# Kernel tuning notes

Measured on AMD Instinct MI355X. Metric: run time of the kernel, lower is better.

## Reference

```python
import jax, jax.numpy as jnp
import numpy as np
from jax import lax

B = 256
C1 = 256          # conv1 channels
NUM_CAPS = 32     # primary capsule types
CAP_DIM = 8       # primary capsule dim
NUM_PRIMARY = NUM_CAPS * 6 * 6  # 1152
NUM_OUT = 10
OUT_DIM = 16
NUM_ROUTING = 3


def squash(v):
    # v: (..., d)
    sq = jnp.sum(v * v, axis=-1, keepdims=True)
    scale = sq / (1.0 + sq)
    return scale * v / jnp.sqrt(sq + 1e-8)


def setup_inputs() -> dict:
    key = jax.random.key(0)
    k = jax.random.split(key, 6)
    x = jax.random.normal(k[0], (B, 1, 28, 28), dtype=jnp.float32)
    # kaiming fan_out init for convs
    conv1_w = jax.random.normal(k[1], (C1, 1, 9, 9), dtype=jnp.float32) * np.sqrt(2.0 / (C1 * 81))
    conv1_b = jnp.zeros((C1,), dtype=jnp.float32)
    pc_out = NUM_CAPS * CAP_DIM  # 256
    pc_w = jax.random.normal(k[2], (pc_out, C1, 9, 9), dtype=jnp.float32) * np.sqrt(2.0 / (pc_out * 81))
    pc_b = jnp.zeros((pc_out,), dtype=jnp.float32)
    W_digit = jax.random.normal(k[3], (NUM_PRIMARY, CAP_DIM, NUM_OUT, OUT_DIM), dtype=jnp.float32) * 0.01
    return {"x": x, "conv1_w": conv1_w, "conv1_b": conv1_b,
            "pc_w": pc_w, "pc_b": pc_b, "W_digit": W_digit}


def _conv(x, w, b, stride):
    y = lax.conv_general_dilated(x, w, (stride, stride), 'VALID',
                                 dimension_numbers=('NCHW', 'OIHW', 'NCHW'))
    return y + b[None, :, None, None]


def reference(x, conv1_w, conv1_b, pc_w, pc_b, W_digit):
    # conv1 + ReLU: (B,1,28,28) -> (B,256,20,20)
    h = jax.nn.relu(_conv(x, conv1_w, conv1_b, 1))
    # primary caps conv: -> (B, 256, 6, 6)
    p = _conv(h, pc_w, pc_b, 2)
    bsz, _, oh, ow = p.shape
    # (B, num_caps, cap_dim, H, W) -> (B, num_caps, H, W, cap_dim) -> (B, N, d)
    p = p.reshape(bsz, NUM_CAPS, CAP_DIM, oh, ow)
    p = jnp.transpose(p, (0, 1, 3, 4, 2)).reshape(bsz, NUM_CAPS * oh * ow, CAP_DIM)
    u = squash(p)  # (B, 1152, 8)
    # dynamic routing
    u_hat = jnp.einsum('bid,idjo->bijo', u, W_digit)  # (B, 1152, 10, 16)
    b_logits = jnp.zeros((bsz, NUM_PRIMARY, NUM_OUT, 1), dtype=u_hat.dtype)
    v = None
    for it in range(NUM_ROUTING):
        c = jax.nn.softmax(b_logits, axis=2)
        s = jnp.sum(c * u_hat, axis=1)          # (B, 10, 16)
        v = squash(s)
        if it < NUM_ROUTING - 1:
            agreement = jnp.sum(u_hat * v[:, None, :, :], axis=-1, keepdims=True)
            b_logits = b_logits + agreement
    return v
```

## Files before the change

### kernel.cpp

```cpp
#include <hip/hip_runtime.h>
#include <hip/hip_bf16.h>

#define NI 1152

typedef __attribute__((ext_vector_type(8))) _Float16 f16x8;
typedef __attribute__((ext_vector_type(4))) float f32x4;
typedef __attribute__((ext_vector_type(8))) unsigned short u16x8;
typedef __attribute__((ext_vector_type(4))) unsigned short u16x4;

static const size_t UHAT_OFF = 0;
static const size_t W6_OFF   = 0;
static const size_t H3_OFF   = 10750976UL;
static const size_t WT1_OFF  = 63179776UL;
static const size_t PP_OFF   = 94371840UL;
static const size_t SP_OFF   = 103809024UL;
static const size_t L_OFF    = 127401984UL;
static const size_t V_OFF    = 139198464UL;

__device__ __forceinline__ unsigned short f2bf(float x) {
    unsigned u = __builtin_bit_cast(unsigned, x);
    u += 0x7fffu + ((u >> 16) & 1u);
    return (unsigned short)(u >> 16);
}
__device__ __forceinline__ float bf2f(unsigned short h) {
    return __builtin_bit_cast(float, (unsigned)h << 16);
}
__device__ __forceinline__ void atomAddF(float* p, float v) {
    __hip_atomic_fetch_add(p, v, __ATOMIC_RELAXED, __HIP_MEMORY_SCOPE_AGENT);
}

#define GLD16(gsrc, ldst)                                                      \
    __builtin_amdgcn_global_load_lds(                                          \
        (__attribute__((address_space(1))) const void*)(gsrc),                 \
        (__attribute__((address_space(3))) void*)(ldst), 16, 0, 0)

__global__ __launch_bounds__(256) void k_prep_w(const float* __restrict__ pcw,
                                                _Float16* __restrict__ w6) {
    __shared__ float sl[5184];
    int oc  = blockIdx.x;
    int ic0 = blockIdx.y * 64;
    const float* src = pcw + (size_t)oc * 20736 + (size_t)ic0 * 81;
    for (int j = threadIdx.x; j < 5184; j += 256) sl[j] = src[j];
    __syncthreads();
    int og = oc >> 4, fr = oc & 15;
    for (int t = threadIdx.x; t < 5184; t += 256) {
        int tap = t >> 6, i = t & 63;
        int ic = ic0 + i;
        int ks = ic >> 5, kch = (ic >> 3) & 3, icl = ic & 7;
        int lane = kch * 16 + fr;
        w6[(((size_t)(tap * 8 + ks) * 16 + og) * 64 + lane) * 8 + icl] =
            (_Float16)sl[i * 81 + tap];
    }
}

__global__ void k_transpose_w1(const float* __restrict__ w, float* __restrict__ wT) {
    int t = blockIdx.x, oc = threadIdx.x;
    wT[t * 256 + oc] = w[oc * 81 + t];
}

__global__ __launch_bounds__(256) void k_conv1(const float* __restrict__ x,
                                               const float* __restrict__ wT1,
                                               const float* __restrict__ bias,
                                               _Float16* __restrict__ h3) {
    __shared__ _Float16 hs[2][20][256];
    int b  = blockIdx.y;
    int rp = blockIdx.x;
    int oc = threadIdx.x;
    int oy0 = rp * 2;
    const float* xb = x + (size_t)b * 784;
    float bv = bias[oc];
    float acc0[20], acc1[20];
#pragma unroll
    for (int i = 0; i < 20; ++i) { acc0[i] = bv; acc1[i] = bv; }
    for (int ky = 0; ky < 9; ++ky) {
        const float* r0 = xb + (oy0 + ky) * 28;
        const float* r1 = r0 + 28;
        float x0[28], x1[28];
#pragma unroll
        for (int c = 0; c < 28; ++c) { x0[c] = r0[c]; x1[c] = r1[c]; }
#pragma unroll
        for (int kx = 0; kx < 9; ++kx) {
            float w = wT1[(ky * 9 + kx) * 256 + oc];
#pragma unroll
            for (int px = 0; px < 20; ++px) {
                acc0[px] += x0[px + kx] * w;
                acc1[px] += x1[px + kx] * w;
            }
        }
    }
#pragma unroll
    for (int px = 0; px < 20; ++px) {
        hs[0][px][oc] = (_Float16)fmaxf(acc0[px], 0.f);
        hs[1][px][oc] = (_Float16)fmaxf(acc1[px], 0.f);
    }
    __syncthreads();
    for (int cid = threadIdx.x; cid < 1280; cid += 256) {
        int kp = cid & 31;
        int pos = cid >> 5;
        int ry = pos / 20, px2 = pos % 20;
        int ks = kp >> 2, p = kp & 3;
        f16x8 val = *(const f16x8*)&hs[ry][px2][ks * 32 + p * 8];
        _Float16* dst = h3 + ((size_t)((ks * 400 + (oy0 + ry) * 20 + px2) * 4 + p) * 256 + b) * 8;
        *(f16x8*)dst = val;
    }
}

__global__ __launch_bounds__(256, 2) void k_conv2_mfma(
    const _Float16* __restrict__ h3, const _Float16* __restrict__ w6,
    float* __restrict__ pp) {
    __shared__ _Float16 As[16384], Bs[8192];
    const int pos = blockIdx.x, nt = blockIdx.y, ks = blockIdx.z;
    const int py = pos / 6, px = pos % 6;
    const int l = threadIdx.x & 63;
    const int w = __builtin_amdgcn_readfirstlane((int)(threadIdx.x >> 6));
    const int wm = w >> 1, wn = w & 1;
    const int kch = l >> 4, fr = l & 15;

    f32x4 acc[8][4];
    const f32x4 z = {0.f, 0.f, 0.f, 0.f};
#pragma unroll
    for (int mi = 0; mi < 8; ++mi)
#pragma unroll
        for (int ni = 0; ni < 4; ++ni) acc[mi][ni] = z;

    const size_t h3base = (size_t)ks * 400 * 8192;

    for (int it = 0; it < 41; ++it) {
        const int t0 = 2 * it, t1 = t0 + 1;
        const int tA1 = (t1 > 80) ? 80 : t1;
#pragma unroll
        for (int tl = 0; tl < 2; ++tl) {
            const int tap  = tl ? t1 : t0;
            const int tapA = tl ? tA1 : t0;
            const int y = 2 * py + tapA / 9, xx = 2 * px + tapA % 9;
            const _Float16* asrc = h3 + h3base + (size_t)(y * 20 + xx) * 8192 + w * 2048 + l * 8;
#pragma unroll
            for (int q = 0; q < 4; ++q)
                GLD16(asrc + q * 512, As + tl * 8192 + w * 2048 + q * 512);
            const _Float16* bsrc = w6 + ((size_t)(tap * 8 + ks) * 16 + nt * 8 + w * 2) * 512 + l * 8;
            GLD16(bsrc,       Bs + tl * 4096 + w * 1024);
            GLD16(bsrc + 512, Bs + tl * 4096 + w * 1024 + 512);
        }
        __syncthreads();
#pragma unroll
        for (int tl = 0; tl < 2; ++tl) {
            const _Float16* Ab = As + tl * 8192 + kch * 2048 + (wm * 128 + fr) * 8;
            const _Float16* Bb = Bs + tl * 4096 + wn * 2048 + kch * 128 + fr * 8;
            f16x8 a[8], b[4];
#pragma unroll
            for (int mi = 0; mi < 8; ++mi) a[mi] = *(const f16x8*)(Ab + mi * 128);
#pragma unroll
            for (int ni = 0; ni < 4; ++ni) b[ni] = *(const f16x8*)(Bb + ni * 512);
#pragma unroll
            for (int mi = 0; mi < 8; ++mi)
#pragma unroll
                for (int ni = 0; ni < 4; ++ni)
                    acc[mi][ni] = __builtin_amdgcn_mfma_f32_16x16x32_f16(a[mi], b[ni], acc[mi][ni], 0, 0, 0);
        }
        __syncthreads();
    }
    const int row0 = kch * 4;
#pragma unroll
    for (int mi = 0; mi < 8; ++mi)
#pragma unroll
        for (int ni = 0; ni < 4; ++ni) {
            int nloc = wn * 64 + ni * 16 + fr;
#pragma unroll
            for (int reg = 0; reg < 4; ++reg) {
                int mloc = wm * 128 + mi * 16 + row0 + reg;
                atomAddF(&pp[((size_t)pos * 256 + mloc) * 256 + nt * 128 + nloc],
                         acc[mi][ni][reg]);
            }
        }
}

__global__ __launch_bounds__(256) void k_postconv(const float* __restrict__ pp,
                                                  const float* __restrict__ bias,
                                                  const float* __restrict__ W,
                                                  unsigned short* __restrict__ UH,
                                                  float* __restrict__ SP) {
    int it = blockIdx.x, bt = blockIdx.y;
    int i0 = it * 8, b0 = bt * 64;
    int og = threadIdx.x & 3, b_l = threadIdx.x >> 2;
    int b = b0 + b_l;
    float acc[10][4];
#pragma unroll
    for (int j = 0; j < 10; ++j)
#pragma unroll
        for (int o = 0; o < 4; ++o) acc[j][o] = 0.f;
#pragma unroll
    for (int li = 0; li < 8; ++li) {
        int i = i0 + li;
        int cap = i / 36, posi = i - cap * 36;
        const float* p0 = pp + ((size_t)posi * 256 + b) * 256 + cap * 8;
        float4 pa = ((const float4*)p0)[0];
        float4 pb = ((const float4*)p0)[1];
        const float* bs = bias + cap * 8;
        float s8[8] = {pa.x + bs[0], pa.y + bs[1], pa.z + bs[2], pa.w + bs[3],
                       pb.x + bs[4], pb.y + bs[5], pb.z + bs[6], pb.w + bs[7]};
        float sq = 0.f;
#pragma unroll
        for (int d = 0; d < 8; ++d) sq += s8[d] * s8[d];
        float scale = sq / ((1.0f + sq) * sqrtf(sq + 1e-8f));
        float u8[8];
#pragma unroll
        for (int d = 0; d < 8; ++d) u8[d] = scale * s8[d];
        const float* Wi = W + (size_t)i * 1280 + og * 4;
#pragma unroll
        for (int j = 0; j < 10; ++j) {
            float o4[4] = {0.f, 0.f, 0.f, 0.f};
#pragma unroll
            for (int d = 0; d < 8; ++d) {
                float4 wv = *(const float4*)(Wi + d * 160 + j * 16);
                o4[0] += u8[d] * wv.x; o4[1] += u8[d] * wv.y;
                o4[2] += u8[d] * wv.z; o4[3] += u8[d] * wv.w;
            }
            u16x4 h;
#pragma unroll
            for (int o = 0; o < 4; ++o) { h[o] = f2bf(o4[o]); acc[j][o] += o4[o]; }
            *(u16x4*)(UH + ((size_t)(i * 10 + j) * 256 + b) * 16 + og * 4) = h;
        }
    }
    float* sp = SP + ((size_t)it * 256 + b) * 160 + og * 4;
#pragma unroll
    for (int j = 0; j < 10; ++j)
        *(float4*)(sp + j * 16) = make_float4(0.1f * acc[j][0], 0.1f * acc[j][1],
                                              0.1f * acc[j][2], 0.1f * acc[j][3]);
}

__global__ __launch_bounds__(256) void k_route_as(float* __restrict__ L,
                                                  const unsigned short* __restrict__ UH,
                                                  const float* __restrict__ V,
                                                  float* __restrict__ SP,
                                                  int add, int storeL) {
    __shared__ float VL[64][165];
    __shared__ float LG[64][81];
    int it = blockIdx.x, bt = blockIdx.y;
    int b0 = bt * 64, i0 = it * 8;
    int b_l = threadIdx.x & 63;
    int ig = __builtin_amdgcn_readfirstlane((int)(threadIdx.x >> 6));
    int b_r = threadIdx.x >> 2, part = threadIdx.x & 3;
    {
        const float4* vsrc = (const float4*)(V + (size_t)(b0 + b_r) * 160 + part * 40);
#pragma unroll
        for (int q = 0; q < 10; ++q) {
            float4 vv = vsrc[q]; int c = part * 40 + q * 4;
            VL[b_r][c] = vv.x; VL[b_r][c + 1] = vv.y; VL[b_r][c + 2] = vv.z; VL[b_r][c + 3] = vv.w;
        }
        if (add) {
            const float4* lsrc = (const float4*)(L + (size_t)(b0 + b_r) * 11520 + i0 * 10 + part * 20);
#pragma unroll
            for (int q = 0; q < 5; ++q) {
                float4 t = lsrc[q]; int c = part * 20 + q * 4;
                LG[b_r][c] = t.x; LG[b_r][c + 1] = t.y; LG[b_r][c + 2] = t.z; LG[b_r][c + 3] = t.w;
            }
        }
    }
    __syncthreads();
#pragma unroll
    for (int ii = 0; ii < 2; ++ii) {
        int il = ig * 2 + ii;
        int i = i0 + il;
        const unsigned short* up = UH + ((size_t)i * 10 * 256 + b0 + b_l) * 16;
#pragma unroll
        for (int j = 0; j < 10; ++j) {
            u16x8 ua = *(const u16x8*)(up + j * 4096);
            u16x8 ub = *(const u16x8*)(up + j * 4096 + 8);
            float a = 0.f;
#pragma unroll
            for (int o = 0; o < 8; ++o) a += bf2f(ua[o]) * VL[b_l][j * 16 + o];
#pragma unroll
            for (int o = 0; o < 8; ++o) a += bf2f(ub[o]) * VL[b_l][j * 16 + 8 + o];
            float base = add ? LG[b_l][il * 10 + j] : 0.f;
            LG[b_l][il * 10 + j] = base + a;
        }
    }
    __syncthreads();
    if (storeL) {
        float4* ldst = (float4*)(L + (size_t)(b0 + b_r) * 11520 + i0 * 10 + part * 20);
#pragma unroll
        for (int q = 0; q < 5; ++q) {
            int c = part * 20 + q * 4;
            ldst[q] = make_float4(LG[b_r][c], LG[b_r][c + 1], LG[b_r][c + 2], LG[b_r][c + 3]);
        }
    }
    float acc[10][4];
#pragma unroll
    for (int j = 0; j < 10; ++j)
#pragma unroll
        for (int o = 0; o < 4; ++o) acc[j][o] = 0.f;
    for (int li = 0; li < 8; ++li) {
        float lg[10];
#pragma unroll
        for (int j = 0; j < 10; ++j) lg[j] = LG[b_l][li * 10 + j];
        float m = lg[0];
#pragma unroll
        for (int j = 1; j < 10; ++j) m = fmaxf(m, lg[j]);
        float e[10], ssum = 0.f;
#pragma unroll
        for (int j = 0; j < 10; ++j) { e[j] = __expf(lg[j] - m); ssum += e[j]; }
        float inv = 1.0f / ssum;
        const unsigned short* up = UH + ((size_t)(i0 + li) * 10 * 256 + b0 + b_l) * 16 + ig * 4;
#pragma unroll
        for (int j = 0; j < 10; ++j) {
            float cj = e[j] * inv;
            u16x4 t = *(const u16x4*)(up + j * 4096);
#pragma unroll
            for (int o = 0; o < 4; ++o) acc[j][o] += cj * bf2f(t[o]);
        }
    }
    float* sp = SP + ((size_t)it * 256 + b0 + b_l) * 160 + ig * 4;
#pragma unroll
    for (int j = 0; j < 10; ++j)
        *(float4*)(sp + j * 16) = make_float4(acc[j][0], acc[j][1], acc[j][2], acc[j][3]);
}

__global__ __launch_bounds__(256) void k_route_v(const float* __restrict__ SP,
                                                 float* __restrict__ vout) {
    int n = blockIdx.x * 256 + threadIdx.x;
    float ssum = 0.f;
    for (int t = 0; t < 144; ++t) ssum += SP[(size_t)t * 40960 + n];
    float sq = ssum * ssum;
    float tot = sq;
#pragma unroll
    for (int mask = 1; mask < 16; mask <<= 1) tot += __shfl_xor(tot, mask, 64);
    float scale = tot / ((1.0f + tot) * sqrtf(tot + 1e-8f));
    vout[n] = scale * ssum;
}

extern "C" void kernel_launch(void* const* d_in, const int* in_sizes, int n_in,
                              void* d_out, int out_size, void* d_ws, size_t ws_size,
                              hipStream_t stream) {
    (void)in_sizes; (void)n_in; (void)out_size; (void)ws_size;
    const float* x   = (const float*)d_in[0];
    const float* c1w = (const float*)d_in[1];
    const float* c1b = (const float*)d_in[2];
    const float* pcw = (const float*)d_in[3];
    const float* pcb = (const float*)d_in[4];
    const float* Wd  = (const float*)d_in[5];
    float* out = (float*)d_out;
    char* wsb  = (char*)d_ws;

    unsigned short* uh = (unsigned short*)(wsb + UHAT_OFF);
    _Float16* w6 = (_Float16*)(wsb + W6_OFF);
    _Float16* h3 = (_Float16*)(wsb + H3_OFF);
    float* wT1 = (float*)(wsb + WT1_OFF);
    float* pp  = (float*)(wsb + PP_OFF);
    float* sp  = (float*)(wsb + SP_OFF);
    float* lg  = (float*)(wsb + L_OFF);
    float* v   = (float*)(wsb + V_OFF);

    hipMemsetAsync(pp, 0, (size_t)9216 * 256 * sizeof(float), stream);
    hipMemsetAsync(w6 + (size_t)81 * 65536, 0, 131072, stream);

    k_prep_w<<<dim3(256, 4), 256, 0, stream>>>(pcw, w6);
    k_transpose_w1<<<81, 256, 0, stream>>>(c1w, wT1);
    k_conv1<<<dim3(10, 256), 256, 0, stream>>>(x, wT1, c1b, h3);
    k_conv2_mfma<<<dim3(36, 2, 8), 256, 0, stream>>>(h3, w6, pp);
    k_postconv<<<dim3(144, 4), 256, 0, stream>>>(pp, pcb, Wd, uh, sp);

    k_route_v<<<160, 256, 0, stream>>>(sp, v);
    k_route_as<<<dim3(144, 4), 256, 0, stream>>>(lg, uh, v, sp, 0, 1);
    k_route_v<<<160, 256, 0, stream>>>(sp, v);
    k_route_as<<<dim3(144, 4), 256, 0, stream>>>(lg, uh, v, sp, 1, 0);
    k_route_v<<<160, 256, 0, stream>>>(sp, out);
}
```

Measured before the change: 523.0 us.

## Halve conv2 MFMA block M-tile and re-layout weights for more blocks

The primary-capsule conv GEMM now splits each output position's 256 batch rows into two 128-row halves. That doubles the grid to 72x2x8 blocks and halves the per-block accumulator and LDS A buffer. The weight pre-layout changes to a row-major-per-chunk format so A and B tiles load with the same LDS offsets. Launch bounds are raised to allow 4 blocks per CU. The aim is more parallelism and occupancy, at the cost of loading each weight tile twice as often and doubling the atomic-add write traffic per element group.

```diff
diff --git a/kernel.cpp b/kernel.cpp
--- a/kernel.cpp
+++ b/kernel.cpp
@@ -9,7 +9,7 @@
 typedef __attribute__((ext_vector_type(4))) unsigned short u16x4;
 
 static const size_t UHAT_OFF = 0;
-static const size_t W6_OFF   = 0;
+static const size_t W5_OFF   = 0;
 static const size_t H3_OFF   = 10750976UL;
 static const size_t WT1_OFF  = 63179776UL;
 static const size_t PP_OFF   = 94371840UL;
@@ -35,20 +35,19 @@
         (__attribute__((address_space(3))) void*)(ldst), 16, 0, 0)
 
 __global__ __launch_bounds__(256) void k_prep_w(const float* __restrict__ pcw,
-                                                _Float16* __restrict__ w6) {
+                                                _Float16* __restrict__ w5) {
     __shared__ float sl[5184];
     int oc  = blockIdx.x;
     int ic0 = blockIdx.y * 64;
     const float* src = pcw + (size_t)oc * 20736 + (size_t)ic0 * 81;
     for (int j = threadIdx.x; j < 5184; j += 256) sl[j] = src[j];
     __syncthreads();
-    int og = oc >> 4, fr = oc & 15;
+    int nt = oc >> 7, row = oc & 127;
     for (int t = threadIdx.x; t < 5184; t += 256) {
         int tap = t >> 6, i = t & 63;
         int ic = ic0 + i;
-        int ks = ic >> 5, kch = (ic >> 3) & 3, icl = ic & 7;
-        int lane = kch * 16 + fr;
-        w6[(((size_t)(tap * 8 + ks) * 16 + og) * 64 + lane) * 8 + icl] =
+        int ks = ic >> 5, p = (ic >> 3) & 3, icl = ic & 7;
+        w5[((size_t)(((tap * 8 + ks) * 2 + nt) * 4 + p) * 128 + row) * 8 + icl] =
             (_Float16)sl[i * 81 + tap];
     }
 }
@@ -105,25 +104,28 @@
     }
 }
 
-__global__ __launch_bounds__(256, 2) void k_conv2_mfma(
-    const _Float16* __restrict__ h3, const _Float16* __restrict__ w6,
+__global__ __launch_bounds__(256, 4) void k_conv2_mfma(
+    const _Float16* __restrict__ h3, const _Float16* __restrict__ w5,
     float* __restrict__ pp) {
-    __shared__ _Float16 As[16384], Bs[8192];
-    const int pos = blockIdx.x, nt = blockIdx.y, ks = blockIdx.z;
+    __shared__ _Float16 As[8192], Bs[8192];
+    const int mt = blockIdx.x, nt = blockIdx.y, ks = blockIdx.z;
+    const int pos = mt >> 1, bhalf = mt & 1;
     const int py = pos / 6, px = pos % 6;
     const int l = threadIdx.x & 63;
     const int w = __builtin_amdgcn_readfirstlane((int)(threadIdx.x >> 6));
     const int wm = w >> 1, wn = w & 1;
-    const int kch = l >> 4, fr = l & 15;
-
-    f32x4 acc[8][4];
+
+    f32x4 acc[4][4];
     const f32x4 z = {0.f, 0.f, 0.f, 0.f};
 #pragma unroll
-    for (int mi = 0; mi < 8; ++mi)
+    for (int mi = 0; mi < 4; ++mi)
 #pragma unroll
         for (int ni = 0; ni < 4; ++ni) acc[mi][ni] = z;
 
-    const size_t h3base = (size_t)ks * 400 * 8192;
+    const int ch = (l >> 4) * 1024;
+    const int am = (wm * 64 + (l & 15)) * 8;
+    const int bn = (wn * 64 + (l & 15)) * 8;
+    const int lds_off = w * 1024 + l * 8;
 
     for (int it = 0; it < 41; ++it) {
         const int t0 = 2 * it, t1 = t0 + 1;
@@ -133,43 +135,43 @@
             const int tap  = tl ? t1 : t0;
             const int tapA = tl ? tA1 : t0;
             const int y = 2 * py + tapA / 9, xx = 2 * px + tapA % 9;
-            const _Float16* asrc = h3 + h3base + (size_t)(y * 20 + xx) * 8192 + w * 2048 + l * 8;
-#pragma unroll
-            for (int q = 0; q < 4; ++q)
-                GLD16(asrc + q * 512, As + tl * 8192 + w * 2048 + q * 512);
-            const _Float16* bsrc = w6 + ((size_t)(tap * 8 + ks) * 16 + nt * 8 + w * 2) * 512 + l * 8;
-            GLD16(bsrc,       Bs + tl * 4096 + w * 1024);
-            GLD16(bsrc + 512, Bs + tl * 4096 + w * 1024 + 512);
+            const _Float16* asrc = h3 + ((size_t)(ks * 400 + y * 20 + xx) * 4 + w) * 2048 +
+                                   bhalf * 1024 + l * 8;
+            const _Float16* bsrc = w5 + ((size_t)((tap * 8 + ks) * 2 + nt)) * 4096 + lds_off;
+            GLD16(asrc,       As + tl * 4096 + lds_off);
+            GLD16(asrc + 512, As + tl * 4096 + lds_off + 512);
+            GLD16(bsrc,       Bs + tl * 4096 + lds_off);
+            GLD16(bsrc + 512, Bs + tl * 4096 + lds_off + 512);
         }
         __syncthreads();
 #pragma unroll
-        for (int tl = 0; tl < 2; ++tl) {
-            const _Float16* Ab = As + tl * 8192 + kch * 2048 + (wm * 128 + fr) * 8;
-            const _Float16* Bb = Bs + tl * 4096 + wn * 2048 + kch * 128 + fr * 8;
-            f16x8 a[8], b[4];
-#pragma unroll
-            for (int mi = 0; mi < 8; ++mi) a[mi] = *(const f16x8*)(Ab + mi * 128);
-#pragma unroll
-            for (int ni = 0; ni < 4; ++ni) b[ni] = *(const f16x8*)(Bb + ni * 512);
-#pragma unroll
-            for (int mi = 0; mi < 8; ++mi)
+        for (int s = 0; s < 2; ++s) {
+            const int pb = s * 4096 + ch;
+            f16x8 a[4], b[4];
+#pragma unroll
+            for (int i = 0; i < 4; ++i) {
+                a[i] = *(const f16x8*)(As + pb + am + i * 128);
+                b[i] = *(const f16x8*)(Bs + pb + bn + i * 128);
+            }
+#pragma unroll
+            for (int mi = 0; mi < 4; ++mi)
 #pragma unroll
                 for (int ni = 0; ni < 4; ++ni)
                     acc[mi][ni] = __builtin_amdgcn_mfma_f32_16x16x32_f16(a[mi], b[ni], acc[mi][ni], 0, 0, 0);
         }
         __syncthreads();
     }
-    const int row0 = kch * 4;
-#pragma unroll
-    for (int mi = 0; mi < 8; ++mi)
+    const int row0 = (l >> 4) * 4;
+    const int ncol = l & 15;
+#pragma unroll
+    for (int mi = 0; mi < 4; ++mi)
 #pragma unroll
         for (int ni = 0; ni < 4; ++ni) {
-            int nloc = wn * 64 + ni * 16 + fr;
+            int n = nt * 128 + wn * 64 + ni * 16 + ncol;
 #pragma unroll
             for (int reg = 0; reg < 4; ++reg) {
-                int mloc = wm * 128 + mi * 16 + row0 + reg;
-                atomAddF(&pp[((size_t)pos * 256 + mloc) * 256 + nt * 128 + nloc],
-                         acc[mi][ni][reg]);
+                int m = pos * 256 + bhalf * 128 + wm * 64 + mi * 16 + row0 + reg;
+                atomAddF(&pp[(size_t)m * 256 + n], acc[mi][ni][reg]);
             }
         }
 }
@@ -342,7 +344,7 @@
     char* wsb  = (char*)d_ws;
 
     unsigned short* uh = (unsigned short*)(wsb + UHAT_OFF);
-    _Float16* w6 = (_Float16*)(wsb + W6_OFF);
+    _Float16* w5 = (_Float16*)(wsb + W5_OFF);
     _Float16* h3 = (_Float16*)(wsb + H3_OFF);
     float* wT1 = (float*)(wsb + WT1_OFF);
     float* pp  = (float*)(wsb + PP_OFF);
@@ -351,12 +353,12 @@
     float* v   = (float*)(wsb + V_OFF);
 
     hipMemsetAsync(pp, 0, (size_t)9216 * 256 * sizeof(float), stream);
-    hipMemsetAsync(w6 + (size_t)81 * 65536, 0, 131072, stream);
-
-    k_prep_w<<<dim3(256, 4), 256, 0, stream>>>(pcw, w6);
+    hipMemsetAsync(w5 + (size_t)81 * 65536, 0, (size_t)65536 * sizeof(_Float16), stream);
+
+    k_prep_w<<<dim3(256, 4), 256, 0, stream>>>(pcw, w5);
     k_transpose_w1<<<81, 256, 0, stream>>>(c1w, wT1);
     k_conv1<<<dim3(10, 256), 256, 0, stream>>>(x, wT1, c1b, h3);
-    k_conv2_mfma<<<dim3(36, 2, 8), 256, 0, stream>>>(h3, w6, pp);
+    k_conv2_mfma<<<dim3(72, 2, 8), 256, 0, stream>>>(h3, w5, pp);
     k_postconv<<<dim3(144, 4), 256, 0, stream>>>(pp, pcb, Wd, uh, sp);
 
     k_route_v<<<160, 256, 0, stream>>>(sp, v);
```

After: 477.2 us. 8.8% less time.
